# Kernel optimization log

Measured on AMD Instinct MI355X. Metric: run time of the kernel, lower is better.

Reference implementation:

```python
import jax, jax.numpy as jnp
import numpy as np

D_MODEL = 512
NUM_HEADS = 8
D_FF = 2048
SEQ = 2048
BATCH = 2
EPS = 1e-5


def _linear(x, W, b):
    # x: [S,B,D_in], W: [D_out, D_in] (torch convention), b: [D_out]
    return jnp.einsum('sbd,ed->sbe', x, W) + b


def _layer_norm(x, g, b):
    mu = jnp.mean(x, axis=-1, keepdims=True)
    var = jnp.var(x, axis=-1, keepdims=True)
    return (x - mu) * jax.lax.rsqrt(var + EPS) * g + b


def _mha(q_in, k_in, v_in, W, b, mask4d, num_heads):
    # q_in: [Sq,B,D], k_in/v_in: [Sk,B,D]; W: [4,D,D], b: [4,D]
    Sq, B, D = q_in.shape
    Sk = k_in.shape[0]
    dk = D // num_heads
    q = _linear(q_in, W[0], b[0]).reshape(Sq, B, num_heads, dk).transpose(1, 2, 0, 3)
    k = _linear(k_in, W[1], b[1]).reshape(Sk, B, num_heads, dk).transpose(1, 2, 0, 3)
    v = _linear(v_in, W[2], b[2]).reshape(Sk, B, num_heads, dk).transpose(1, 2, 0, 3)
    scores = jnp.einsum('bhqd,bhkd->bhqk', q, k) / jnp.sqrt(jnp.asarray(dk, q.dtype))
    scores = jnp.where(mask4d, -jnp.inf, scores)
    p = jax.nn.softmax(scores, axis=-1)  # dropout p=0 -> identity
    o = jnp.einsum('bhqk,bhkd->bhqd', p, v)  # [B,H,Sq,dk]
    o = o.transpose(2, 0, 1, 3).reshape(Sq, B, D)
    return _linear(o, W[3], b[3])


def setup_inputs() -> dict:
    key = jax.random.key(0)
    ks = jax.random.split(key, 12)
    scale = 1.0 / np.sqrt(D_MODEL)
    inp = {
        'x': jax.random.normal(ks[0], (SEQ, BATCH, D_MODEL), jnp.float32),
        'memory': jax.random.normal(ks[1], (SEQ, BATCH, D_MODEL), jnp.float32),
        # causal mask: True = masked (strictly upper triangular)
        'tgt_mask': jnp.triu(jnp.ones((SEQ, SEQ), dtype=bool), k=1),
        # per-batch key padding mask for cross attention
        'memory_mask': jax.random.randint(ks[2], (BATCH, SEQ), 0, 2) > 0,
        'sa_W': jax.random.normal(ks[3], (4, D_MODEL, D_MODEL), jnp.float32) * scale,
        'sa_b': jnp.zeros((4, D_MODEL), jnp.float32),
        'ca_W': jax.random.normal(ks[4], (4, D_MODEL, D_MODEL), jnp.float32) * scale,
        'ca_b': jnp.zeros((4, D_MODEL), jnp.float32),
        'w1': jax.random.normal(ks[5], (D_FF, D_MODEL), jnp.float32) * scale,
        'b1': jnp.zeros((D_FF,), jnp.float32),
        'w2': jax.random.normal(ks[6], (D_MODEL, D_FF), jnp.float32) * (1.0 / np.sqrt(D_FF)),
        'b2': jnp.zeros((D_MODEL,), jnp.float32),
        'ln_g': jnp.ones((3, D_MODEL), jnp.float32),
        'ln_b': jnp.zeros((3, D_MODEL), jnp.float32),
    }
    return inp


def reference(x, memory, tgt_mask, memory_mask, sa_W, sa_b, ca_W, ca_b,
              w1, b1, w2, b2, ln_g, ln_b):
    # self-attention block (pre-norm, residual)
    nx = _layer_norm(x, ln_g[0], ln_b[0])
    sa = _mha(nx, nx, nx, sa_W, sa_b, tgt_mask[None, None], NUM_HEADS)
    x = x + sa
    # cross-attention block
    nx = _layer_norm(x, ln_g[1], ln_b[1])
    ca = _mha(nx, memory, memory, ca_W, ca_b, memory_mask[:, None, None, :], NUM_HEADS)
    x = x + ca
    # FFN block
    nx = _layer_norm(x, ln_g[2], ln_b[2])
    ff = _linear(jax.nn.relu(_linear(nx, w1, b1)), w2, b2)
    return x + ff
```

## Files before the change

### kernel.cpp

```cpp
#include <hip/hip_runtime.h>

#define S_LEN 2048
#define BATCH_N 2
#define DM 512
#define H_N 8
#define DK_N 64
#define FF_N 2048
#define M_TOK (S_LEN*BATCH_N)
#define QSZ (BATCH_N*H_N*S_LEN*DK_N)
#define MN_PART 2097152

typedef __attribute__((ext_vector_type(8))) short short8;
typedef __attribute__((ext_vector_type(4))) float f32x4;
typedef __attribute__((ext_vector_type(16))) float f32x16;
typedef __attribute__((ext_vector_type(4))) unsigned uint4v;

__device__ __forceinline__ unsigned short f2b(float f) {
  union { float f; unsigned u; } v; v.f = f;
  unsigned r = v.u + 0x7FFFu + ((v.u >> 16) & 1u);
  return (unsigned short)(r >> 16);
}
__device__ __forceinline__ float b2f(unsigned short u) {
  union { unsigned u; float f; } v; v.u = ((unsigned)u) << 16; return v.f;
}

__device__ __forceinline__ void gl_lds16(const void* g, void* l) {
  __builtin_amdgcn_global_load_lds(
      (__attribute__((address_space(1))) unsigned int*)(unsigned long long)g,
      (__attribute__((address_space(3))) unsigned int*)(unsigned int)(unsigned long long)l,
      16, 0, 0);
}

__device__ __forceinline__ void cast4(const float* __restrict__ src,
                                      unsigned short* __restrict__ dst, int i) {
  float4 v = *(const float4*)(src + i);
  ushort4 o; o.x = f2b(v.x); o.y = f2b(v.y); o.z = f2b(v.z); o.w = f2b(v.w);
  *(ushort4*)(dst + i) = o;
}

__device__ __forceinline__ void ln_row_wave(const float* __restrict__ in,
    const float* __restrict__ g, const float* __restrict__ b,
    unsigned short* __restrict__ out, int row, int lane) {
  const float4* src = (const float4*)(in + (size_t)row * DM);
  float4 v0 = src[lane*2], v1 = src[lane*2 + 1];
  float s  = v0.x+v0.y+v0.z+v0.w + v1.x+v1.y+v1.z+v1.w;
  float ss = v0.x*v0.x+v0.y*v0.y+v0.z*v0.z+v0.w*v0.w
           + v1.x*v1.x+v1.y*v1.y+v1.z*v1.z+v1.w*v1.w;
  #pragma unroll
  for (int off = 32; off >= 1; off >>= 1) {
    s  += __shfl_xor(s,  off);
    ss += __shfl_xor(ss, off);
  }
  float mean = s * (1.f/512.f);
  float inv  = rsqrtf(ss * (1.f/512.f) - mean*mean + 1e-5f);
  float4 g0 = ((const float4*)g)[lane*2], g1 = ((const float4*)g)[lane*2 + 1];
  float4 b0 = ((const float4*)b)[lane*2], b1 = ((const float4*)b)[lane*2 + 1];
  ushort4 o0, o1;
  o0.x = f2b((v0.x-mean)*inv*g0.x + b0.x);
  o0.y = f2b((v0.y-mean)*inv*g0.y + b0.y);
  o0.z = f2b((v0.z-mean)*inv*g0.z + b0.z);
  o0.w = f2b((v0.w-mean)*inv*g0.w + b0.w);
  o1.x = f2b((v1.x-mean)*inv*g1.x + b1.x);
  o1.y = f2b((v1.y-mean)*inv*g1.y + b1.y);
  o1.z = f2b((v1.z-mean)*inv*g1.z + b1.z);
  o1.w = f2b((v1.w-mean)*inv*g1.w + b1.w);
  ushort4* dst = (ushort4*)(out + (size_t)row * DM);
  dst[lane*2]     = o0;
  dst[lane*2 + 1] = o1;
}

__global__ __launch_bounds__(256) void prep_kernel(
    const float* __restrict__ sa_W, const float* __restrict__ ca_W,
    const float* __restrict__ w1, const float* __restrict__ w2,
    const float* __restrict__ memory, const int* __restrict__ mm,
    const float* __restrict__ x, const float* __restrict__ ln_g,
    const float* __restrict__ ln_b,
    unsigned short* __restrict__ o_sa, unsigned short* __restrict__ o_ca,
    unsigned short* __restrict__ o_w1, unsigned short* __restrict__ o_w2,
    unsigned short* __restrict__ o_mem, unsigned long long* __restrict__ bmo,
    unsigned short* __restrict__ nx)
{
  int blk = blockIdx.x, t = threadIdx.x;
  if (blk < 1024)      cast4(sa_W, o_sa, (blk*256 + t)*4);
  else if (blk < 2048) cast4(ca_W, o_ca, ((blk-1024)*256 + t)*4);
  else if (blk < 3072) cast4(w1,   o_w1, ((blk-2048)*256 + t)*4);
  else if (blk < 4096) cast4(w2,   o_w2, ((blk-3072)*256 + t)*4);
  else if (blk < 6144) cast4(memory, o_mem, ((blk-4096)*256 + t)*4);
  else if (blk == 6144) {
    if (t < 64) {
      int b = t >> 5, kt = t & 31;
      unsigned long long m = 0ull;
      for (int j = 0; j < 64; j++)
        m |= (unsigned long long)(mm[b*S_LEN + kt*64 + j] != 0) << j;
      bmo[b*32 + kt] = m;
    }
  } else {
    int row = (blk - 6145)*4 + (t >> 6);
    ln_row_wave(x, ln_g, ln_b, nx, row, t & 63);
  }
}

__global__ __launch_bounds__(256) void ln4_kernel(const float* __restrict__ in,
                                                  const float* __restrict__ g,
                                                  const float* __restrict__ b,
                                                  unsigned short* __restrict__ out) {
  ln_row_wave(in, g, b, out, blockIdx.x*4 + (threadIdx.x >> 6), threadIdx.x & 63);
}

template<int RELU, int OUTMODE, int RESID>
__global__ __launch_bounds__(256) void gemm_bt(
    const unsigned short* __restrict__ A, const unsigned short* __restrict__ W,
    const float* __restrict__ bias, const float* __restrict__ resid,
    float* __restrict__ Cf, unsigned short* __restrict__ Cb,
    int M, int N, int K, int Kstride)
{
  __shared__ unsigned short As[2][64*40];
  __shared__ unsigned short Bs[2][64*40];
  int tid = threadIdx.x;
  int lane = tid & 63, w = tid >> 6;
  int wr = w >> 1, wc = w & 1;
  int bm = blockIdx.y * 64, bn = blockIdx.x * 64;
  int kz = blockIdx.z;
  f32x4 acc[2][2] = {};
  int lrow = tid >> 2;
  int lcg  = (tid & 3) * 8;
  const size_t aoff = (size_t)(bm + lrow) * Kstride + (size_t)kz * K + lcg;
  const size_t boff = (size_t)(bn + lrow) * Kstride + (size_t)kz * K + lcg;
  int fr = lane & 15, kg = (lane >> 4) * 8;
  short8 pa = *(const short8*)&A[aoff];
  short8 pb = *(const short8*)&W[boff];
  *(short8*)&As[0][lrow*40 + lcg] = pa;
  *(short8*)&Bs[0][lrow*40 + lcg] = pb;
  __syncthreads();
  int cur = 0;
  for (int k0 = 0; k0 < K; k0 += 32) {
    bool hn = (k0 + 32) < K;
    if (hn) {
      pa = *(const short8*)&A[aoff + k0 + 32];
      pb = *(const short8*)&W[boff + k0 + 32];
    }
    short8 af0 = *(const short8*)&As[cur][(wr*32 +      fr)*40 + kg];
    short8 af1 = *(const short8*)&As[cur][(wr*32 + 16 + fr)*40 + kg];
    short8 bf0 = *(const short8*)&Bs[cur][(wc*32 +      fr)*40 + kg];
    short8 bf1 = *(const short8*)&Bs[cur][(wc*32 + 16 + fr)*40 + kg];
    acc[0][0] = __builtin_amdgcn_mfma_f32_16x16x32_bf16(af0, bf0, acc[0][0], 0,0,0);
    acc[0][1] = __builtin_amdgcn_mfma_f32_16x16x32_bf16(af0, bf1, acc[0][1], 0,0,0);
    acc[1][0] = __builtin_amdgcn_mfma_f32_16x16x32_bf16(af1, bf0, acc[1][0], 0,0,0);
    acc[1][1] = __builtin_amdgcn_mfma_f32_16x16x32_bf16(af1, bf1, acc[1][1], 0,0,0);
    if (hn) {
      *(short8*)&As[cur^1][lrow*40 + lcg] = pa;
      *(short8*)&Bs[cur^1][lrow*40 + lcg] = pb;
    }
    __syncthreads();
    cur ^= 1;
  }
  int rbase = (lane >> 4) * 4;
  #pragma unroll
  for (int m = 0; m < 2; m++) {
    #pragma unroll
    for (int n = 0; n < 2; n++) {
      int col = bn + wc*32 + n*16 + (lane & 15);
      float bc = (OUTMODE == 3) ? 0.f : bias[col];
      #pragma unroll
      for (int r = 0; r < 4; r++) {
        int row = bm + wr*32 + m*16 + rbase + r;
        float vv = acc[m][n][r] + bc;
        if (RELU) vv = fmaxf(vv, 0.f);
        if (OUTMODE == 2) {
          int which = col >> 9, hh = (col >> 6) & 7, dd = col & 63;
          if (which == 0) vv *= 0.125f;
          size_t idx = ((((size_t)which*BATCH_N + (row & 1))*H_N + hh)*S_LEN + (row >> 1))*DK_N + dd;
          Cb[idx] = f2b(vv);
        } else if (OUTMODE == 3) {
          Cf[(size_t)kz*MN_PART + (size_t)row*N + col] = vv;
        } else {
          size_t idx = (size_t)row * N + col;
          if (RESID) vv += resid[idx];
          if (OUTMODE == 1) Cb[idx] = f2b(vv);
          else              Cf[idx] = vv;
        }
      }
    }
  }
}

__global__ __launch_bounds__(256) void ffn2_combine(
    const float* __restrict__ part, const float* __restrict__ bias,
    const float* __restrict__ resid, float* __restrict__ out)
{
  int i = (blockIdx.x*256 + threadIdx.x)*4;
  float4 a = *(const float4*)(part + i);
  float4 b = *(const float4*)(part + MN_PART + i);
  float4 bs = *(const float4*)(bias + (i & 511));
  float4 rs = *(const float4*)(resid + i);
  float4 o;
  o.x = a.x + b.x + bs.x + rs.x;
  o.y = a.y + b.y + bs.y + rs.y;
  o.z = a.z + b.z + bs.z + rs.z;
  o.w = a.w + b.w + bs.w + rs.w;
  *(float4*)(out + i) = o;
}

template<int RELU, int OUTMODE, int VSTART>
__global__ __launch_bounds__(256) void gemm128(
    const unsigned short* __restrict__ A, const unsigned short* __restrict__ W,
    const float* __restrict__ bias, unsigned short* __restrict__ Cb,
    int M, int N, int K)
{
  __shared__ unsigned short As[128*32];
  __shared__ unsigned short Bs[128*32];
  int tid = threadIdx.x, lane = tid & 63, w = tid >> 6;
  int bm = blockIdx.y * 128, bn = blockIdx.x * 128;
  int fr = lane & 15, hi = lane >> 4;
  int kg8 = hi*8, rg = hi*4;
  int wm = (w >> 1) * 64, wn = (w & 1) * 64;
  f32x4 acc[4][4] = {};
  const unsigned short* ga0 = A + (size_t)(bm +      (tid>>2))*K + (tid&3)*8;
  const unsigned short* ga1 = A + (size_t)(bm + 64 + (tid>>2))*K + (tid&3)*8;
  const unsigned short* gb0 = W + (size_t)(bn +      (tid>>2))*K + (tid&3)*8;
  const unsigned short* gb1 = W + (size_t)(bn + 64 + (tid>>2))*K + (tid&3)*8;
  unsigned short* lA0 = &As[tid*8];
  unsigned short* lA1 = &As[2048 + tid*8];
  unsigned short* lB0 = &Bs[tid*8];
  unsigned short* lB1 = &Bs[2048 + tid*8];
  for (int k0 = 0; k0 < K; k0 += 32) {
    gl_lds16(ga0 + k0, lA0);
    gl_lds16(ga1 + k0, lA1);
    gl_lds16(gb0 + k0, lB0);
    gl_lds16(gb1 + k0, lB1);
    __syncthreads();
    short8 af[4], bf[4];
    #pragma unroll
    for (int m = 0; m < 4; m++) af[m] = *(const short8*)&As[(wm + m*16 + fr)*32 + kg8];
    #pragma unroll
    for (int n = 0; n < 4; n++) bf[n] = *(const short8*)&Bs[(wn + n*16 + fr)*32 + kg8];
    __builtin_amdgcn_s_setprio(1);
    #pragma unroll
    for (int m = 0; m < 4; m++)
      #pragma unroll
      for (int n = 0; n < 4; n++)
        acc[m][n] = __builtin_amdgcn_mfma_f32_16x16x32_bf16(af[m], bf[n], acc[m][n], 0,0,0);
    __builtin_amdgcn_s_setprio(0);
    __syncthreads();
  }
  #pragma unroll
  for (int m = 0; m < 4; m++) {
    #pragma unroll
    for (int n = 0; n < 4; n++) {
      int col = bn + wn + n*16 + fr;
      float bc = bias[col];
      #pragma unroll
      for (int r = 0; r < 4; r++) {
        int row = bm + wm + m*16 + rg + r;
        float vv = acc[m][n][r] + bc;
        if (RELU) vv = fmaxf(vv, 0.f);
        if (OUTMODE == 2) {
          int which = col >> 9, hh = (col >> 6) & 7, dd = col & 63;
          int srow = row >> 1, bb = row & 1;
          size_t idx;
          if (which >= VSTART)
            idx = (size_t)which*QSZ + (((size_t)bb*H_N + hh)*DK_N + dd)*S_LEN + srow;
          else
            idx = (size_t)which*QSZ + (((size_t)bb*H_N + hh)*S_LEN + srow)*DK_N + dd;
          Cb[idx] = f2b(vv);
        } else {
          Cb[(size_t)row * N + col] = f2b(vv);
        }
      }
    }
  }
}

__global__ __launch_bounds__(256) void gemm128_dual(
    const unsigned short* __restrict__ A0, const unsigned short* __restrict__ W0,
    const float* __restrict__ bias0, unsigned short* __restrict__ C0,
    const unsigned short* __restrict__ A1, const unsigned short* __restrict__ W1,
    const float* __restrict__ bias1, unsigned short* __restrict__ C1)
{
  const int K = 512;
  int bx = blockIdx.x;
  const unsigned short* A; const unsigned short* W; const float* bias;
  unsigned short* Cb; int bn, vs;
  if (bx < 12) { A = A0; W = W0; bias = bias0; Cb = C0; bn = bx*128;      vs = 2; }
  else         { A = A1; W = W1; bias = bias1; Cb = C1; bn = (bx-12)*128; vs = 1; }
  __shared__ unsigned short As[128*32];
  __shared__ unsigned short Bs[128*32];
  int tid = threadIdx.x, lane = tid & 63, w = tid >> 6;
  int bm = blockIdx.y * 128;
  int fr = lane & 15, hi = lane >> 4;
  int kg8 = hi*8, rg = hi*4;
  int wm = (w >> 1) * 64, wn = (w & 1) * 64;
  f32x4 acc[4][4] = {};
  const unsigned short* ga0 = A + (size_t)(bm +      (tid>>2))*K + (tid&3)*8;
  const unsigned short* ga1 = A + (size_t)(bm + 64 + (tid>>2))*K + (tid&3)*8;
  const unsigned short* gb0 = W + (size_t)(bn +      (tid>>2))*K + (tid&3)*8;
  const unsigned short* gb1 = W + (size_t)(bn + 64 + (tid>>2))*K + (tid&3)*8;
  unsigned short* lA0 = &As[tid*8];
  unsigned short* lA1 = &As[2048 + tid*8];
  unsigned short* lB0 = &Bs[tid*8];
  unsigned short* lB1 = &Bs[2048 + tid*8];
  for (int k0 = 0; k0 < K; k0 += 32) {
    gl_lds16(ga0 + k0, lA0);
    gl_lds16(ga1 + k0, lA1);
    gl_lds16(gb0 + k0, lB0);
    gl_lds16(gb1 + k0, lB1);
    __syncthreads();
    short8 af[4], bf[4];
    #pragma unroll
    for (int m = 0; m < 4; m++) af[m] = *(const short8*)&As[(wm + m*16 + fr)*32 + kg8];
    #pragma unroll
    for (int n = 0; n < 4; n++) bf[n] = *(const short8*)&Bs[(wn + n*16 + fr)*32 + kg8];
    __builtin_amdgcn_s_setprio(1);
    #pragma unroll
    for (int m = 0; m < 4; m++)
      #pragma unroll
      for (int n = 0; n < 4; n++)
        acc[m][n] = __builtin_amdgcn_mfma_f32_16x16x32_bf16(af[m], bf[n], acc[m][n], 0,0,0);
    __builtin_amdgcn_s_setprio(0);
    __syncthreads();
  }
  #pragma unroll
  for (int m = 0; m < 4; m++) {
    #pragma unroll
    for (int n = 0; n < 4; n++) {
      int col = bn + wn + n*16 + fr;
      float bc = bias[col];
      #pragma unroll
      for (int r = 0; r < 4; r++) {
        int row = bm + wm + m*16 + rg + r;
        float vv = acc[m][n][r] + bc;
        int which = col >> 9, hh = (col >> 6) & 7, dd = col & 63;
        if (vs == 2 && which == 0) vv *= 0.125f;
        int srow = row >> 1, bb = row & 1;
        size_t idx;
        if (which >= vs)
          idx = (size_t)which*QSZ + (((size_t)bb*H_N + hh)*DK_N + dd)*S_LEN + srow;
        else
          idx = (size_t)which*QSZ + (((size_t)bb*H_N + hh)*S_LEN + srow)*DK_N + dd;
        Cb[idx] = f2b(vv);
      }
    }
  }
}

template<int MODE>
__global__ __launch_bounds__(256, 4) void attn3(
    const unsigned short* __restrict__ qg, const unsigned short* __restrict__ kpl,
    const unsigned short* __restrict__ vtpl, const unsigned long long* __restrict__ bm,
    unsigned short* __restrict__ opart, float* __restrict__ lpart)
{
  __shared__ unsigned short SM[2*64*72];
  unsigned short* Ks = SM;
  unsigned short* Vt = SM + 64*72;
  int tid = threadIdx.x;
  int lane = tid & 63, w = tid >> 6;
  int l31 = lane & 31, hi5 = lane >> 5;
  int bid = blockIdx.x;
  int p = bid & 15, u = bid >> 4;
  int qtile = u >> 2, range = u & 3;
  int h = p & 7, b = p >> 3;
  const size_t sbase = (size_t)(b*H_N + h) * S_LEN;
  int kt0 = range*8, kt1 = kt0 + 7;
  if (MODE == 0) {
    if (kt0 > qtile*2 + 1) return;
    if (kt1 > qtile*2 + 1) kt1 = qtile*2 + 1;
  }
  int wbase = qtile*128 + w*32;
  int ktw = (wbase + 31) >> 6;
  int qrow = wbase + l31;
  short8 qf[4];
  #pragma unroll
  for (int km = 0; km < 4; km++)
    qf[km] = *(const short8*)&qg[(sbase + qrow)*DK_N + km*16 + hi5*8];

  int sr = tid >> 2, sc = (tid & 3) * 16;
  const unsigned short* kbase = &kpl[(sbase + sr)*DK_N + sc];
  const unsigned short* vbase = &vtpl[((size_t)(b*H_N + h)*DK_N + sr)*S_LEN + sc];

  f32x16 oa0 = {}, oa1 = {};
  float lp = 0.f;
  for (int kt = kt0; kt <= kt1; kt++) {
    __syncthreads();
    {
      const unsigned short* kg = kbase + (size_t)kt*64*DK_N;
      const unsigned short* vg = vbase + kt*64;
      *(short8*)&Ks[sr*72 + sc]     = *(const short8*)kg;
      *(short8*)&Ks[sr*72 + sc + 8] = *(const short8*)(kg + 8);
      *(short8*)&Vt[sr*72 + sc]     = *(const short8*)vg;
      *(short8*)&Vt[sr*72 + sc + 8] = *(const short8*)(vg + 8);
    }
    __syncthreads();
    if (MODE == 0 && kt > ktw) continue;
    bool dmask = (MODE == 0) && (kt == ktw);
    #pragma unroll
    for (int kb = 0; kb < 2; kb++) {
      f32x16 sa = {};
      __builtin_amdgcn_s_setprio(1);
      #pragma unroll
      for (int km = 0; km < 4; km++) {
        short8 kf = *(const short8*)&Ks[(kb*32 + l31)*72 + km*16 + hi5*8];
        sa = __builtin_amdgcn_mfma_f32_32x32x16_bf16(kf, qf[km], sa, 0, 0, 0);
      }
      __builtin_amdgcn_s_setprio(0);
      float pv[16];
      float psum = 0.f;
      if (MODE == 1) {
        unsigned mlo = (unsigned)(bm[b*32 + kt] >> (kb*32 + 4*hi5));
        #pragma unroll
        for (int r = 0; r < 16; r++) {
          const int pos = (r & 3) + 8*(r >> 2);
          float e = __expf(sa[r]);
          if ((mlo >> pos) & 1u) e = 0.f;
          pv[r] = e; psum += e;
        }
      } else if (dmask) {
        #pragma unroll
        for (int r = 0; r < 16; r++) {
          const int pos = (r & 3) + 8*(r >> 2);
          float e = __expf(sa[r]);
          if (kt*64 + kb*32 + 4*hi5 + pos > qrow) e = 0.f;
          pv[r] = e; psum += e;
        }
      } else {
        #pragma unroll
        for (int r = 0; r < 16; r++) {
          float e = __expf(sa[r]);
          pv[r] = e; psum += e;
        }
      }
      lp += psum;
      unsigned pk[8];
      #pragma unroll
      for (int i = 0; i < 8; i++)
        asm("v_cvt_pk_bf16_f32 %0, %1, %2" : "=v"(pk[i]) : "v"(pv[2*i]), "v"(pv[2*i+1]));
      asm("v_permlane32_swap_b32 %0, %1" : "+v"(pk[0]), "+v"(pk[2]));
      asm("v_permlane32_swap_b32 %0, %1" : "+v"(pk[1]), "+v"(pk[3]));
      asm("v_permlane32_swap_b32 %0, %1" : "+v"(pk[4]), "+v"(pk[6]));
      asm("v_permlane32_swap_b32 %0, %1" : "+v"(pk[5]), "+v"(pk[7]));
      uint4v f0v, f1v;
      f0v.x = pk[0]; f0v.y = pk[1]; f0v.z = pk[2]; f0v.w = pk[3];
      f1v.x = pk[4]; f1v.y = pk[5]; f1v.z = pk[6]; f1v.w = pk[7];
      short8 pf0 = *(short8*)&f0v;
      short8 pf1 = *(short8*)&f1v;
      __builtin_amdgcn_s_setprio(1);
      {
        short8 v00 = *(const short8*)&Vt[(     l31)*72 + kb*32 +      hi5*8];
        short8 v01 = *(const short8*)&Vt[(     l31)*72 + kb*32 + 16 + hi5*8];
        oa0 = __builtin_amdgcn_mfma_f32_32x32x16_bf16(pf0, v00, oa0, 0, 0, 0);
        oa0 = __builtin_amdgcn_mfma_f32_32x32x16_bf16(pf1, v01, oa0, 0, 0, 0);
        short8 v10 = *(const short8*)&Vt[(32 + l31)*72 + kb*32 +      hi5*8];
        short8 v11 = *(const short8*)&Vt[(32 + l31)*72 + kb*32 + 16 + hi5*8];
        oa1 = __builtin_amdgcn_mfma_f32_32x32x16_bf16(pf0, v10, oa1, 0, 0, 0);
        oa1 = __builtin_amdgcn_mfma_f32_32x32x16_bf16(pf1, v11, oa1, 0, 0, 0);
      }
      __builtin_amdgcn_s_setprio(0);
    }
  }
  float lptot = lp + __shfl_xor(lp, 32);
  if (lane < 32)
    lpart[((size_t)sbase + wbase + l31)*4 + range] = lptot;
  #pragma unroll
  for (int r = 0; r < 16; r++) {
    const int pos = (r & 3) + 8*(r >> 2);
    int qr = wbase + pos + 4*hi5;
    size_t obase = (size_t)range*QSZ + (sbase + (size_t)qr)*DK_N;
    opart[obase + l31]      = f2b(oa0[r]);
    opart[obase + 32 + l31] = f2b(oa1[r]);
  }
}

template<int CAUSAL>
__global__ __launch_bounds__(256) void attn_combine4(
    const unsigned short* __restrict__ op, const float* __restrict__ lp,
    unsigned short* __restrict__ o)
{
  int t = blockIdx.x*256 + threadIdx.x;
  int f = t*8;
  int col = f & 511, row = f >> 9;
  int h = col >> 6, d = col & 63, s = row >> 1, b = row & 1;
  size_t pr = ((size_t)b*H_N + h)*S_LEN + s;
  size_t base = pr*DK_N + d;
  int nact = CAUSAL ? ((s >> 9) + 1) : 4;
  float4 lv = *(const float4*)(lp + pr*4);
  float l = lv.x;
  if (!CAUSAL || nact > 1) l += lv.y;
  if (!CAUSAL || nact > 2) l += lv.z;
  if (!CAUSAL || nact > 3) l += lv.w;
  float acc[8] = {0.f,0.f,0.f,0.f,0.f,0.f,0.f,0.f};
  #pragma unroll
  for (int r = 0; r < 4; r++) {
    if (!CAUSAL || r < nact) {
      short8 a = *(const short8*)&op[(size_t)r*QSZ + base];
      #pragma unroll
      for (int i = 0; i < 8; i++) acc[i] += b2f((unsigned short)a[i]);
    }
  }
  float inv = 1.f / l;
  short8 r8;
  #pragma unroll
  for (int i = 0; i < 8; i++) r8[i] = (short)f2b(acc[i] * inv);
  *(short8*)&o[(size_t)row*DM + col] = r8;
}

extern "C" void kernel_launch(void* const* d_in, const int* in_sizes, int n_in,
                              void* d_out, int out_size, void* d_ws, size_t ws_size,
                              hipStream_t stream) {
  const float* x       = (const float*)d_in[0];
  const float* memory  = (const float*)d_in[1];
  const int*   memmask = (const int*)d_in[3];
  const float* sa_W = (const float*)d_in[4];
  const float* sa_b = (const float*)d_in[5];
  const float* ca_W = (const float*)d_in[6];
  const float* ca_b = (const float*)d_in[7];
  const float* w1   = (const float*)d_in[8];
  const float* b1   = (const float*)d_in[9];
  const float* w2   = (const float*)d_in[10];
  const float* b2   = (const float*)d_in[11];
  const float* ln_g = (const float*)d_in[12];
  const float* ln_b = (const float*)d_in[13];
  float* out = (float*)d_out;

  char* ws = (char*)d_ws;
  float*          xcur   = (float*)ws;
  unsigned short* nx_bf  = (unsigned short*)(ws + (8u<<20));
  unsigned short* qkv_sa = (unsigned short*)(ws + (12u<<20));
  unsigned short* q_ca   = (unsigned short*)(ws + (24u<<20));
  unsigned short* kv_ca  = (unsigned short*)(ws + (28u<<20));
  unsigned short* o_bf   = (unsigned short*)(ws + (36u<<20));
  unsigned short* mem_bf = (unsigned short*)(ws + (40u<<20));
  unsigned short* h_bf   = (unsigned short*)(ws + (44u<<20));
  unsigned short* opart  = (unsigned short*)(ws + (44u<<20));
  float*          fpart  = (float*)(ws + (12u<<20));
  float*          lpart  = (float*)(ws + (60u<<20));
  unsigned long long* bmsk = (unsigned long long*)(ws + (60u<<20) + (1u<<19));
  unsigned short* w_sa   = (unsigned short*)(ws + (61u<<20));
  unsigned short* w_ca   = w_sa + 4*512*512;
  unsigned short* w_f1   = w_ca + 4*512*512;
  unsigned short* w_f2   = w_f1 + 2048*512;

  dim3 blk(256);
  dim3 g512 (512/64,  4096/64);
  dim3 gdual(20, 4096/128);
  dim3 q128_2048(2048/128, 4096/128);
  dim3 gsplitk(512/64, 4096/64, 2);

  prep_kernel<<<7169, blk, 0, stream>>>(sa_W, ca_W, w1, w2, memory, memmask,
                                        x, ln_g, ln_b,
                                        w_sa, w_ca, w_f1, w_f2, mem_bf, bmsk, nx_bf);

  gemm128_dual<<<gdual, blk, 0, stream>>>(nx_bf, w_sa, sa_b, qkv_sa,
                                          mem_bf, w_ca + 262144, ca_b + 512, kv_ca);
  attn3<0><<<1024, blk, 0, stream>>>(qkv_sa, qkv_sa + QSZ, qkv_sa + 2*QSZ, nullptr, opart, lpart);
  attn_combine4<1><<<1024, blk, 0, stream>>>(opart, lpart, o_bf);
  gemm_bt<0,0,1><<<g512, blk, 0, stream>>>(o_bf, w_sa + 3*262144, sa_b + 1536, x, xcur, nullptr, 4096, 512, 512, 512);

  ln4_kernel<<<1024, blk, 0, stream>>>(xcur, ln_g + 512, ln_b + 512, nx_bf);
  gemm_bt<0,2,0><<<g512, blk, 0, stream>>>(nx_bf, w_ca, ca_b, nullptr, nullptr, q_ca, 4096, 512, 512, 512);
  attn3<1><<<1024, blk, 0, stream>>>(q_ca, kv_ca, kv_ca + QSZ, bmsk, opart, lpart);
  attn_combine4<0><<<1024, blk, 0, stream>>>(opart, lpart, o_bf);
  gemm_bt<0,0,1><<<g512, blk, 0, stream>>>(o_bf, w_ca + 3*262144, ca_b + 1536, xcur, xcur, nullptr, 4096, 512, 512, 512);

  ln4_kernel<<<1024, blk, 0, stream>>>(xcur, ln_g + 1024, ln_b + 1024, nx_bf);
  gemm128<1,1,0><<<q128_2048, blk, 0, stream>>>(nx_bf, w_f1, b1, h_bf, 4096, 2048, 512);
  gemm_bt<0,3,0><<<gsplitk, blk, 0, stream>>>(h_bf, w_f2, nullptr, nullptr, fpart, nullptr, 4096, 512, 1024, 2048);
  ffn2_combine<<<2048, blk, 0, stream>>>(fpart, b2, xcur, out);
}
```

Measured before the change: 186.4 us.

## Use 128-key attention tiles and store FFN2 split-K partials in bf16

The attention kernel now stages 128 keys per iteration instead of 64, which halves the number of barrier-separated load phases. Causal skipping moves to 32-key sub-blocks, and each range covers 4 of the larger tiles. Separately, the FFN2 split-K partial sums are written as bf16 instead of fp32 and the combine kernel reads 8 elements per thread, cutting partial-buffer traffic. The costs are larger LDS use per block, which can hurt occupancy, and extra rounding error in the FFN partials.

```diff
diff --git a/kernel.cpp b/kernel.cpp
--- a/kernel.cpp
+++ b/kernel.cpp
@@ -172,7 +172,7 @@
           size_t idx = ((((size_t)which*BATCH_N + (row & 1))*H_N + hh)*S_LEN + (row >> 1))*DK_N + dd;
           Cb[idx] = f2b(vv);
         } else if (OUTMODE == 3) {
-          Cf[(size_t)kz*MN_PART + (size_t)row*N + col] = vv;
+          Cb[(size_t)kz*MN_PART + (size_t)row*N + col] = f2b(vv);
         } else {
           size_t idx = (size_t)row * N + col;
           if (RESID) vv += resid[idx];
@@ -185,20 +185,27 @@
 }
 
 __global__ __launch_bounds__(256) void ffn2_combine(
-    const float* __restrict__ part, const float* __restrict__ bias,
+    const unsigned short* __restrict__ part, const float* __restrict__ bias,
     const float* __restrict__ resid, float* __restrict__ out)
 {
-  int i = (blockIdx.x*256 + threadIdx.x)*4;
-  float4 a = *(const float4*)(part + i);
-  float4 b = *(const float4*)(part + MN_PART + i);
-  float4 bs = *(const float4*)(bias + (i & 511));
-  float4 rs = *(const float4*)(resid + i);
-  float4 o;
-  o.x = a.x + b.x + bs.x + rs.x;
-  o.y = a.y + b.y + bs.y + rs.y;
-  o.z = a.z + b.z + bs.z + rs.z;
-  o.w = a.w + b.w + bs.w + rs.w;
-  *(float4*)(out + i) = o;
+  int i = (blockIdx.x*256 + threadIdx.x)*8;
+  short8 a = *(const short8*)&part[i];
+  short8 b = *(const short8*)&part[MN_PART + i];
+  float4 bs0 = *(const float4*)(bias + (i & 511));
+  float4 bs1 = *(const float4*)(bias + ((i & 511) + 4));
+  float4 rs0 = *(const float4*)(resid + i);
+  float4 rs1 = *(const float4*)(resid + i + 4);
+  float4 o0, o1;
+  o0.x = b2f((unsigned short)a[0]) + b2f((unsigned short)b[0]) + bs0.x + rs0.x;
+  o0.y = b2f((unsigned short)a[1]) + b2f((unsigned short)b[1]) + bs0.y + rs0.y;
+  o0.z = b2f((unsigned short)a[2]) + b2f((unsigned short)b[2]) + bs0.z + rs0.z;
+  o0.w = b2f((unsigned short)a[3]) + b2f((unsigned short)b[3]) + bs0.w + rs0.w;
+  o1.x = b2f((unsigned short)a[4]) + b2f((unsigned short)b[4]) + bs1.x + rs1.x;
+  o1.y = b2f((unsigned short)a[5]) + b2f((unsigned short)b[5]) + bs1.y + rs1.y;
+  o1.z = b2f((unsigned short)a[6]) + b2f((unsigned short)b[6]) + bs1.z + rs1.z;
+  o1.w = b2f((unsigned short)a[7]) + b2f((unsigned short)b[7]) + bs1.w + rs1.w;
+  *(float4*)(out + i)     = o0;
+  *(float4*)(out + i + 4) = o1;
 }
 
 template<int RELU, int OUTMODE, int VSTART>
@@ -344,14 +351,13 @@
 }
 
 template<int MODE>
-__global__ __launch_bounds__(256, 4) void attn3(
+__global__ __launch_bounds__(256, 4) void attn4(
     const unsigned short* __restrict__ qg, const unsigned short* __restrict__ kpl,
     const unsigned short* __restrict__ vtpl, const unsigned long long* __restrict__ bm,
     unsigned short* __restrict__ opart, float* __restrict__ lpart)
 {
-  __shared__ unsigned short SM[2*64*72];
-  unsigned short* Ks = SM;
-  unsigned short* Vt = SM + 64*72;
+  __shared__ unsigned short Ks[128*72];
+  __shared__ unsigned short Vt[64*136];
   int tid = threadIdx.x;
   int lane = tid & 63, w = tid >> 6;
   int l31 = lane & 31, hi5 = lane >> 5;
@@ -360,40 +366,43 @@
   int qtile = u >> 2, range = u & 3;
   int h = p & 7, b = p >> 3;
   const size_t sbase = (size_t)(b*H_N + h) * S_LEN;
-  int kt0 = range*8, kt1 = kt0 + 7;
+  int kt0 = range*4, kt1 = kt0 + 3;
   if (MODE == 0) {
-    if (kt0 > qtile*2 + 1) return;
-    if (kt1 > qtile*2 + 1) kt1 = qtile*2 + 1;
+    if (kt0 > qtile) return;
+    if (kt1 > qtile) kt1 = qtile;
   }
   int wbase = qtile*128 + w*32;
-  int ktw = (wbase + 31) >> 6;
   int qrow = wbase + l31;
   short8 qf[4];
   #pragma unroll
   for (int km = 0; km < 4; km++)
     qf[km] = *(const short8*)&qg[(sbase + qrow)*DK_N + km*16 + hi5*8];
 
-  int sr = tid >> 2, sc = (tid & 3) * 16;
-  const unsigned short* kbase = &kpl[(sbase + sr)*DK_N + sc];
-  const unsigned short* vbase = &vtpl[((size_t)(b*H_N + h)*DK_N + sr)*S_LEN + sc];
+  int krow = tid >> 1, kc0 = (tid & 1) * 32;
+  int vd   = tid >> 2, vc0 = (tid & 3) * 32;
+  const unsigned short* kbase = &kpl[(sbase + krow)*DK_N + kc0];
+  const unsigned short* vbase = &vtpl[((size_t)(b*H_N + h)*DK_N + vd)*S_LEN + vc0];
 
   f32x16 oa0 = {}, oa1 = {};
   float lp = 0.f;
   for (int kt = kt0; kt <= kt1; kt++) {
     __syncthreads();
     {
-      const unsigned short* kg = kbase + (size_t)kt*64*DK_N;
-      const unsigned short* vg = vbase + kt*64;
-      *(short8*)&Ks[sr*72 + sc]     = *(const short8*)kg;
-      *(short8*)&Ks[sr*72 + sc + 8] = *(const short8*)(kg + 8);
-      *(short8*)&Vt[sr*72 + sc]     = *(const short8*)vg;
-      *(short8*)&Vt[sr*72 + sc + 8] = *(const short8*)(vg + 8);
-    }
-    __syncthreads();
-    if (MODE == 0 && kt > ktw) continue;
-    bool dmask = (MODE == 0) && (kt == ktw);
-    #pragma unroll
-    for (int kb = 0; kb < 2; kb++) {
+      const unsigned short* kg = kbase + (size_t)kt*128*DK_N;
+      #pragma unroll
+      for (int j = 0; j < 4; j++)
+        *(short8*)&Ks[krow*72 + kc0 + j*8] = *(const short8*)(kg + j*8);
+      const unsigned short* vg = vbase + kt*128;
+      #pragma unroll
+      for (int j = 0; j < 4; j++)
+        *(short8*)&Vt[vd*136 + vc0 + j*8] = *(const short8*)(vg + j*8);
+    }
+    __syncthreads();
+    #pragma unroll
+    for (int kb = 0; kb < 4; kb++) {
+      int kstart = kt*128 + kb*32;
+      if (MODE == 0 && kstart > wbase + 31) continue;
+      bool dmask = (MODE == 0) && (kstart + 31 > wbase);
       f32x16 sa = {};
       __builtin_amdgcn_s_setprio(1);
       #pragma unroll
@@ -405,7 +414,7 @@
       float pv[16];
       float psum = 0.f;
       if (MODE == 1) {
-        unsigned mlo = (unsigned)(bm[b*32 + kt] >> (kb*32 + 4*hi5));
+        unsigned mlo = (unsigned)(bm[b*32 + kt*2 + (kb>>1)] >> ((kb&1)*32 + 4*hi5));
         #pragma unroll
         for (int r = 0; r < 16; r++) {
           const int pos = (r & 3) + 8*(r >> 2);
@@ -418,7 +427,7 @@
         for (int r = 0; r < 16; r++) {
           const int pos = (r & 3) + 8*(r >> 2);
           float e = __expf(sa[r]);
-          if (kt*64 + kb*32 + 4*hi5 + pos > qrow) e = 0.f;
+          if (kstart + 4*hi5 + pos > qrow) e = 0.f;
           pv[r] = e; psum += e;
         }
       } else {
@@ -444,12 +453,12 @@
       short8 pf1 = *(short8*)&f1v;
       __builtin_amdgcn_s_setprio(1);
       {
-        short8 v00 = *(const short8*)&Vt[(     l31)*72 + kb*32 +      hi5*8];
-        short8 v01 = *(const short8*)&Vt[(     l31)*72 + kb*32 + 16 + hi5*8];
+        short8 v00 = *(const short8*)&Vt[(     l31)*136 + kb*32 +      hi5*8];
+        short8 v01 = *(const short8*)&Vt[(     l31)*136 + kb*32 + 16 + hi5*8];
         oa0 = __builtin_amdgcn_mfma_f32_32x32x16_bf16(pf0, v00, oa0, 0, 0, 0);
         oa0 = __builtin_amdgcn_mfma_f32_32x32x16_bf16(pf1, v01, oa0, 0, 0, 0);
-        short8 v10 = *(const short8*)&Vt[(32 + l31)*72 + kb*32 +      hi5*8];
-        short8 v11 = *(const short8*)&Vt[(32 + l31)*72 + kb*32 + 16 + hi5*8];
+        short8 v10 = *(const short8*)&Vt[(32 + l31)*136 + kb*32 +      hi5*8];
+        short8 v11 = *(const short8*)&Vt[(32 + l31)*136 + kb*32 + 16 + hi5*8];
         oa1 = __builtin_amdgcn_mfma_f32_32x32x16_bf16(pf0, v10, oa1, 0, 0, 0);
         oa1 = __builtin_amdgcn_mfma_f32_32x32x16_bf16(pf1, v11, oa1, 0, 0, 0);
       }
@@ -530,7 +539,7 @@
   unsigned short* mem_bf = (unsigned short*)(ws + (40u<<20));
   unsigned short* h_bf   = (unsigned short*)(ws + (44u<<20));
   unsigned short* opart  = (unsigned short*)(ws + (44u<<20));
-  float*          fpart  = (float*)(ws + (12u<<20));
+  unsigned short* fpart  = (unsigned short*)(ws + (12u<<20));
   float*          lpart  = (float*)(ws + (60u<<20));
   unsigned long long* bmsk = (unsigned long long*)(ws + (60u<<20) + (1u<<19));
   unsigned short* w_sa   = (unsigned short*)(ws + (61u<<20));
@@ -550,18 +559,18 @@
 
   gemm128_dual<<<gdual, blk, 0, stream>>>(nx_bf, w_sa, sa_b, qkv_sa,
                                           mem_bf, w_ca + 262144, ca_b + 512, kv_ca);
-  attn3<0><<<1024, blk, 0, stream>>>(qkv_sa, qkv_sa + QSZ, qkv_sa + 2*QSZ, nullptr, opart, lpart);
+  attn4<0><<<1024, blk, 0, stream>>>(qkv_sa, qkv_sa + QSZ, qkv_sa + 2*QSZ, nullptr, opart, lpart);
   attn_combine4<1><<<1024, blk, 0, stream>>>(opart, lpart, o_bf);
   gemm_bt<0,0,1><<<g512, blk, 0, stream>>>(o_bf, w_sa + 3*262144, sa_b + 1536, x, xcur, nullptr, 4096, 512, 512, 512);
 
   ln4_kernel<<<1024, blk, 0, stream>>>(xcur, ln_g + 512, ln_b + 512, nx_bf);
   gemm_bt<0,2,0><<<g512, blk, 0, stream>>>(nx_bf, w_ca, ca_b, nullptr, nullptr, q_ca, 4096, 512, 512, 512);
-  attn3<1><<<1024, blk, 0, stream>>>(q_ca, kv_ca, kv_ca + QSZ, bmsk, opart, lpart);
+  attn4<1><<<1024, blk, 0, stream>>>(q_ca, kv_ca, kv_ca + QSZ, bmsk, opart, lpart);
   attn_combine4<0><<<1024, blk, 0, stream>>>(opart, lpart, o_bf);
   gemm_bt<0,0,1><<<g512, blk, 0, stream>>>(o_bf, w_ca + 3*262144, ca_b + 1536, xcur, xcur, nullptr, 4096, 512, 512, 512);
 
   ln4_kernel<<<1024, blk, 0, stream>>>(xcur, ln_g + 1024, ln_b + 1024, nx_bf);
   gemm128<1,1,0><<<q128_2048, blk, 0, stream>>>(nx_bf, w_f1, b1, h_bf, 4096, 2048, 512);
-  gemm_bt<0,3,0><<<gsplitk, blk, 0, stream>>>(h_bf, w_f2, nullptr, nullptr, fpart, nullptr, 4096, 512, 1024, 2048);
-  ffn2_combine<<<2048, blk, 0, stream>>>(fpart, b2, xcur, out);
-}
+  gemm_bt<0,3,0><<<gsplitk, blk, 0, stream>>>(h_bf, w_f2, nullptr, nullptr, nullptr, fpart, 4096, 512, 1024, 2048);
+  ffn2_combine<<<1024, blk, 0, stream>>>(fpart, b2, xcur, out);
+}
```

New measurement: 198.3 us. +6.4%, slower.
